# Performance work log

Measured on AMD Instinct MI355X. Metric: run time of the kernel, lower is better.

The kernel has to match this reference:

```python
import jax, jax.numpy as jnp
import numpy as np
from jax import lax

# LRN hyperparameters (from module __init__)
K = 2.0
KERNEL = 5
ALPHA = 1e-4
BETA = 0.75
PAD = KERNEL // 2


def setup_inputs() -> dict:
    key = jax.random.key(0)
    x = jax.random.normal(key, (16, 96, 224, 224), dtype=jnp.float32)
    return {"x": x}


def reference(x) -> jnp.ndarray:
    # Spatial local response norm: per-channel k x k box sum of squares
    # (equivalent to Unfold(kernel, pad=kernel//2) -> view -> square -> sum over window).
    sq = x * x
    ssq = lax.reduce_window(
        sq,
        jnp.float32(0.0),
        lax.add,
        window_dimensions=(1, 1, KERNEL, KERNEL),
        window_strides=(1, 1, 1, 1),
        padding=((0, 0), (0, 0), (PAD, PAD), (PAD, PAD)),
    )
    denom = (K + ALPHA * ssq) ** BETA
    return x / denom
```

## Files before the change

### kernel.cpp

```cpp
#include <hip/hip_runtime.h>


typedef float f4 __attribute__((ext_vector_type(4)));

#define LRN_H 224
#define LRN_W 224
#define LRN_WQ 56
#define LRN_ROWS 28
#define LRN_PLANE (LRN_H * LRN_W)

__device__ __forceinline__ f4 lrn_ld(const float* __restrict__ p) {
    return *(const f4*)p;
}

__device__ __forceinline__ f4 lrn_rowsum_sh(f4 xc, bool okL, bool okR, float mV) {
    f4 sq = xc * xc;
    float a  = __shfl_up(sq[2], 1);
    float b  = __shfl_up(sq[3], 1);
    float d0 = __shfl_down(sq[0], 1);
    float d1 = __shfl_down(sq[1], 1);
    a  = okL ? a  : 0.0f;
    b  = okL ? b  : 0.0f;
    d0 = okR ? d0 : 0.0f;
    d1 = okR ? d1 : 0.0f;
    float t = sq[1] + sq[2];
    f4 r;
    r[0] = (a + b + sq[0] + t) * mV;
    r[1] = (b + sq[0] + t + sq[3]) * mV;
    r[2] = (sq[0] + t + sq[3] + d0) * mV;
    r[3] = (t + sq[3] + d0 + d1) * mV;
    return r;
}

__global__ __launch_bounds__(256) void LocalResponseNorm_17420387352942_kernel(
        const float* __restrict__ x, float* __restrict__ out) {
    const int q   = threadIdx.x;
    const int qe  = min(q, LRN_WQ - 1);
    const int job = blockIdx.x * 4 + threadIdx.y;
    const int plane = job >> 3;
    const int strip = job & 7;
    const int s0    = strip * LRN_ROWS;

    const float* __restrict__ px = x   + (size_t)plane * LRN_PLANE + (qe << 2);
    float* __restrict__       po = out + (size_t)plane * LRN_PLANE + (qe << 2);

    const bool okL = (qe > 0);
    const bool okR = (qe < LRN_WQ - 1);
    const bool wr  = (q < LRN_WQ);

    f4 x0 = lrn_ld(px + max(s0 - 2, 0) * LRN_W);
    f4 x1 = lrn_ld(px + max(s0 - 1, 0) * LRN_W);
    f4 x2 = lrn_ld(px + s0 * LRN_W);
    f4 x3 = lrn_ld(px + (s0 + 1) * LRN_W);
    f4 r0 = lrn_rowsum_sh(x0, okL, okR, (s0 - 2 >= 0) ? 1.0f : 0.0f);
    f4 r1 = lrn_rowsum_sh(x1, okL, okR, (s0 - 1 >= 0) ? 1.0f : 0.0f);
    f4 r2 = lrn_rowsum_sh(x2, okL, okR, 1.0f);
    f4 r3 = lrn_rowsum_sh(x3, okL, okR, 1.0f);
    f4 c0 = x2, c1 = x3;

    f4 A0 = lrn_ld(px + min(s0 + 2, LRN_H - 1) * LRN_W);
    f4 A1 = lrn_ld(px + min(s0 + 3, LRN_H - 1) * LRN_W);
    f4 A2 = lrn_ld(px + min(s0 + 4, LRN_H - 1) * LRN_W);

#pragma unroll
    for (int i = 0; i < LRN_ROWS; ++i) {
        const int h = s0 + i;

        f4 cur = (i % 3 == 0) ? A0 : (i % 3 == 1) ? A1 : A2;
        const float mV = (h + 2 < LRN_H) ? 1.0f : 0.0f;
        f4 r4 = lrn_rowsum_sh(cur, okL, okR, mV);

        {
            f4 nxt = lrn_ld(px + min(h + 5, LRN_H - 1) * LRN_W);
            if (i % 3 == 0) A0 = nxt; else if (i % 3 == 1) A1 = nxt; else A2 = nxt;
        }

        f4 s = r0 + r1 + r2 + r3 + r4;

        f4 o;
#pragma unroll
        for (int j = 0; j < 4; ++j) {
            float d  = fmaf(1e-4f, s[j], 2.0f);
            float rs = __builtin_amdgcn_rsqf(d);
            o[j] = c0[j] * rs * __builtin_amdgcn_sqrtf(rs);
        }
        if (wr) __builtin_nontemporal_store(o, (f4*)(po + h * LRN_W));

        r0 = r1; r1 = r2; r2 = r3; r3 = r4;
        c0 = c1; c1 = cur;
    }
}

extern "C" void kernel_launch(void* const* d_in, const int* in_sizes, int n_in,
                              void* d_out, int out_size, void* d_ws, size_t ws_size,
                              hipStream_t stream) {
    const float* x = (const float*)d_in[0];
    float* out = (float*)d_out;
    dim3 block(64, 4, 1);
    dim3 grid(3072, 1, 1);
    LocalResponseNorm_17420387352942_kernel<<<grid, block, 0, stream>>>(x, out);
}
```

Measured before the change: 516.9 us.

## Split planes into 8-row slabs, load all rows upfront, replace shuffles with neighbor loads

Each wave now handles an 8-row slab instead of a 28-row strip, which raises the number of waves in flight. All 12 input rows needed by a slab are loaded up front, so the rolling prefetch pipeline goes away. The cross-lane shuffles for horizontal neighbours are replaced by extra overlapping vector loads of the left and right float4, with edge masks applied as multipliers. The trade-off is more redundant global and cache reads (halo rows re-read per slab, three loads per row) in exchange for more parallelism and memory-level concurrency.

```diff
diff --git a/kernel.cpp b/kernel.cpp
--- a/kernel.cpp
+++ b/kernel.cpp
@@ -6,88 +6,81 @@
 #define LRN_H 224
 #define LRN_W 224
 #define LRN_WQ 56
-#define LRN_ROWS 28
+#define LRN_R 8
+#define LRN_JOBS_PER_PLANE (LRN_H / LRN_R)
 #define LRN_PLANE (LRN_H * LRN_W)
 
 __device__ __forceinline__ f4 lrn_ld(const float* __restrict__ p) {
     return *(const f4*)p;
 }
 
-__device__ __forceinline__ f4 lrn_rowsum_sh(f4 xc, bool okL, bool okR, float mV) {
-    f4 sq = xc * xc;
-    float a  = __shfl_up(sq[2], 1);
-    float b  = __shfl_up(sq[3], 1);
-    float d0 = __shfl_down(sq[0], 1);
-    float d1 = __shfl_down(sq[1], 1);
-    a  = okL ? a  : 0.0f;
-    b  = okL ? b  : 0.0f;
-    d0 = okR ? d0 : 0.0f;
-    d1 = okR ? d1 : 0.0f;
-    float t = sq[1] + sq[2];
+__device__ __forceinline__ f4 lrn_hsum(f4 xl, f4 xc, f4 xr,
+                                       float mL, float mR, float mV) {
+    float a  = xl[2] * xl[2] * mL;
+    float b  = xl[3] * xl[3] * mL;
+    float c0 = xc[0] * xc[0];
+    float c1 = xc[1] * xc[1];
+    float c2 = xc[2] * xc[2];
+    float c3 = xc[3] * xc[3];
+    float d0 = xr[0] * xr[0] * mR;
+    float d1 = xr[1] * xr[1] * mR;
+    float t = c1 + c2;
     f4 r;
-    r[0] = (a + b + sq[0] + t) * mV;
-    r[1] = (b + sq[0] + t + sq[3]) * mV;
-    r[2] = (sq[0] + t + sq[3] + d0) * mV;
-    r[3] = (t + sq[3] + d0 + d1) * mV;
+    r[0] = (a + b + c0 + t) * mV;
+    r[1] = (b + c0 + t + c3) * mV;
+    r[2] = (c0 + t + c3 + d0) * mV;
+    r[3] = (t + c3 + d0 + d1) * mV;
     return r;
 }
 
-__global__ __launch_bounds__(256) void LocalResponseNorm_17420387352942_kernel(
+__global__ __launch_bounds__(256, 4) void LocalResponseNorm_17420387352942_kernel(
         const float* __restrict__ x, float* __restrict__ out) {
-    const int q   = threadIdx.x;
-    const int qe  = min(q, LRN_WQ - 1);
-    const int job = blockIdx.x * 4 + threadIdx.y;
-    const int plane = job >> 3;
-    const int strip = job & 7;
-    const int s0    = strip * LRN_ROWS;
+    const int q    = threadIdx.x & 63;
+    const int wave = threadIdx.x >> 6;
+    const int job  = blockIdx.x * 4 + wave;
+    const int plane = job / LRN_JOBS_PER_PLANE;
+    const int slab  = job - plane * LRN_JOBS_PER_PLANE;
+    const int h0    = slab * LRN_R;
 
+    const int qe = min(q, LRN_WQ - 1);
     const float* __restrict__ px = x   + (size_t)plane * LRN_PLANE + (qe << 2);
     float* __restrict__       po = out + (size_t)plane * LRN_PLANE + (qe << 2);
 
-    const bool okL = (qe > 0);
-    const bool okR = (qe < LRN_WQ - 1);
+    const float mL = (qe > 0)          ? 1.0f : 0.0f;
+    const float mR = (qe < LRN_WQ - 1) ? 1.0f : 0.0f;
+    const int offL = (qe > 0)          ? -4 : 0;
+    const int offR = (qe < LRN_WQ - 1) ?  4 : 0;
     const bool wr  = (q < LRN_WQ);
 
-    f4 x0 = lrn_ld(px + max(s0 - 2, 0) * LRN_W);
-    f4 x1 = lrn_ld(px + max(s0 - 1, 0) * LRN_W);
-    f4 x2 = lrn_ld(px + s0 * LRN_W);
-    f4 x3 = lrn_ld(px + (s0 + 1) * LRN_W);
-    f4 r0 = lrn_rowsum_sh(x0, okL, okR, (s0 - 2 >= 0) ? 1.0f : 0.0f);
-    f4 r1 = lrn_rowsum_sh(x1, okL, okR, (s0 - 1 >= 0) ? 1.0f : 0.0f);
-    f4 r2 = lrn_rowsum_sh(x2, okL, okR, 1.0f);
-    f4 r3 = lrn_rowsum_sh(x3, okL, okR, 1.0f);
-    f4 c0 = x2, c1 = x3;
-
-    f4 A0 = lrn_ld(px + min(s0 + 2, LRN_H - 1) * LRN_W);
-    f4 A1 = lrn_ld(px + min(s0 + 3, LRN_H - 1) * LRN_W);
-    f4 A2 = lrn_ld(px + min(s0 + 4, LRN_H - 1) * LRN_W);
+    f4 rs[LRN_R + 4];
+    f4 cen[LRN_R];
 
 #pragma unroll
-    for (int i = 0; i < LRN_ROWS; ++i) {
-        const int h = s0 + i;
+    for (int r = 0; r < LRN_R + 4; ++r) {
+        const int row = h0 + r - 2;
+        float mV = 1.0f;
+        int rc = row;
+        if (r < 2)      { mV = (row >= 0)     ? 1.0f : 0.0f; rc = max(row, 0); }
+        else if (r > 9) { mV = (row < LRN_H)  ? 1.0f : 0.0f; rc = min(row, LRN_H - 1); }
+        const float* rp = px + rc * LRN_W;
+        f4 xc = lrn_ld(rp);
+        f4 xl = lrn_ld(rp + offL);
+        f4 xr = lrn_ld(rp + offR);
+        rs[r] = lrn_hsum(xl, xc, xr, mL, mR, mV);
+        if (r >= 2 && r < 2 + LRN_R) cen[r - 2] = xc;
+    }
 
-        f4 cur = (i % 3 == 0) ? A0 : (i % 3 == 1) ? A1 : A2;
-        const float mV = (h + 2 < LRN_H) ? 1.0f : 0.0f;
-        f4 r4 = lrn_rowsum_sh(cur, okL, okR, mV);
-
-        {
-            f4 nxt = lrn_ld(px + min(h + 5, LRN_H - 1) * LRN_W);
-            if (i % 3 == 0) A0 = nxt; else if (i % 3 == 1) A1 = nxt; else A2 = nxt;
-        }
-
-        f4 s = r0 + r1 + r2 + r3 + r4;
-
+#pragma unroll
+    for (int i = 0; i < LRN_R; ++i) {
+        f4 s = rs[i] + rs[i + 1] + rs[i + 2] + rs[i + 3] + rs[i + 4];
         f4 o;
 #pragma unroll
         for (int j = 0; j < 4; ++j) {
             float d  = fmaf(1e-4f, s[j], 2.0f);
-            float rs = __builtin_amdgcn_rsqf(d);
-            o[j] = c0[j] * rs * __builtin_amdgcn_sqrtf(rs);
+            float rsq = __builtin_amdgcn_rsqf(d);
+            o[j] = cen[i][j] * rsq * __builtin_amdgcn_sqrtf(rsq);
         }
-        if (wr) __builtin_nontemporal_store(o, (f4*)(po + h * LRN_W));
-
-        r0 = r1; r1 = r2; r2 = r3; r3 = r4;
-        c0 = c1; c1 = cur;
+        if (wr) __builtin_nontemporal_store(o, (f4*)(po + (h0 + i) * LRN_W));
     }
 }
 
@@ -96,7 +89,7 @@
                               hipStream_t stream) {
     const float* x = (const float*)d_in[0];
     float* out = (float*)d_out;
-    dim3 block(64, 4, 1);
-    dim3 grid(3072, 1, 1);
+    dim3 block(256, 1, 1);
+    dim3 grid(43008 / 4, 1, 1);
     LocalResponseNorm_17420387352942_kernel<<<grid, block, 0, stream>>>(x, out);
 }
```

Result: faster. 496.0 us (-4.0%).
